# Performance work log

Hardware: AMD Instinct MI355X
Metric: run time of the kernel (lower is better)

The kernel has to match this reference:

```python
import jax, jax.numpy as jnp
import numpy as np

B, IN_F, N_HID = 2048, 512, 2048
HEAD = N_HID + IN_F  # 2560


def setup_inputs() -> dict:
    key = jax.random.key(0)
    ks = jax.random.split(key, 14)
    scale = 1.0 / np.sqrt(HEAD)
    # sparsity mask: original [IN_F, N_HID] in {-1,0,1}; _prep_mask pads with
    # ones [N_HID, N_HID], transposes, abs -> [N_HID, HEAD] of {0,1}
    raw = jax.random.randint(ks[0], (IN_F, N_HID), -1, 2).astype(jnp.float32)
    mask = jnp.abs(jnp.concatenate([raw, jnp.ones((N_HID, N_HID), jnp.float32)], axis=0).T)
    def w(k):
        return jax.random.normal(k, (N_HID, HEAD), jnp.float32) * scale
    def b(k):
        return jax.random.normal(k, (N_HID,), jnp.float32) * scale
    return {
        "x": jax.random.normal(ks[1], (B, IN_F), jnp.float32),
        "hidden": jax.random.normal(ks[2], (B, N_HID), jnp.float32),
        "mask": mask,
        "Wg": w(ks[3]), "bg": b(ks[4]),
        "Wh": w(ks[5]), "bh": b(ks[6]),
        "Wfg": w(ks[7]), "bfg": b(ks[8]),
        "Wfh": w(ks[9]), "bfh": b(ks[10]),
        "Wp": w(ks[11]), "bp": b(ks[12]),
    }


def reference(x, hidden, mask, Wg, bg, Wh, bh, Wfg, bfg, Wfh, bfh, Wp, bp):
    # concatenated input shared by all 5 masked linears: [B, HEAD]
    xc = jnp.concatenate([x, hidden], axis=1)
    # fuse the 5 masked GEMMs into one: [5, N_HID, HEAD] stacked weights
    W_all = jnp.stack([Wg, Wh, Wfg, Wfh, Wp]) * mask[None]
    b_all = jnp.stack([bg, bh, bfg, bfh, bp])
    outs = jnp.einsum('bh,koh->kbo', xc, W_all) + b_all[:, None, :]  # [5, B, N_HID]
    g_out, h_out, fg_out, fh_out, p_out = outs
    g = jnp.tanh(g_out)
    h = jnp.tanh(h_out)
    gate = jax.nn.sigmoid(fg_out + fh_out)
    new_hidden = g * (1.0 - gate) + gate * h
    y_pred = p_out + new_hidden
    return (y_pred, new_hidden)
```

## Files before the change

### kernel.cpp

```cpp
#include <hip/hip_runtime.h>

#define MDIM 2048
#define KD   2560
#define NHID 2048
#define INF  512
#define NS   40

typedef __attribute__((ext_vector_type(16))) float f32x16;
typedef __attribute__((ext_vector_type(8))) short short8;
typedef __attribute__((ext_vector_type(8))) unsigned short ushort8v;
typedef __attribute__((ext_vector_type(4))) unsigned short ushort4v;

#define AS1 __attribute__((address_space(1)))
#define AS3 __attribute__((address_space(3)))

__device__ __forceinline__ unsigned short f2bf(float f) {
    unsigned u = __float_as_uint(f);
    u += 0x7fffu + ((u >> 16) & 1u);
    return (unsigned short)(u >> 16);
}

#define XCB 2560
__global__ void prep_all(const float* __restrict__ x, const float* __restrict__ h,
                         unsigned short* __restrict__ xc,
                         const float* __restrict__ Wg, const float* __restrict__ Wh,
                         const float* __restrict__ Wfg, const float* __restrict__ Wfh,
                         const float* __restrict__ Wp, const float* __restrict__ mask,
                         unsigned short* __restrict__ Wm) {
    if (blockIdx.x < XCB) {
        int idx = blockIdx.x * 256 + threadIdx.x;
        int e = idx * 8;
        int b = e / KD;
        int c = e - b * KD;
        const float* src = (c < INF) ? (x + (size_t)b * INF + c)
                                     : (h + (size_t)b * NHID + (c - INF));
        float4 v0 = *(const float4*)src;
        float4 v1 = *(const float4*)(src + 4);
        ushort8v o;
        o[0] = f2bf(v0.x); o[1] = f2bf(v0.y); o[2] = f2bf(v0.z); o[3] = f2bf(v0.w);
        o[4] = f2bf(v1.x); o[5] = f2bf(v1.y); o[6] = f2bf(v1.z); o[7] = f2bf(v1.w);
        *(ushort8v*)(xc + e) = o;
    } else {
        int idx = (blockIdx.x - XCB) * 256 + threadIdx.x;
        size_t e = (size_t)idx * 4;
        const size_t PL = (size_t)NHID * KD;
        int col = (int)(e % KD);
        float4 m;
        if (col < INF) m = *(const float4*)(mask + e);
        else           m = make_float4(1.f, 1.f, 1.f, 1.f);
        const float* Ws[5] = {Wg, Wh, Wfg, Wfh, Wp};
        #pragma unroll
        for (int k = 0; k < 5; ++k) {
            float4 w = *(const float4*)(Ws[k] + e);
            ushort4v o;
            o[0] = f2bf(w.x * m.x); o[1] = f2bf(w.y * m.y);
            o[2] = f2bf(w.z * m.z); o[3] = f2bf(w.w * m.w);
            *(ushort4v*)(Wm + k * PL + e) = o;
        }
    }
}

#define MFMA32(d, va, vb) d = __builtin_amdgcn_mfma_f32_32x32x16_bf16(va, vb, d, 0, 0, 0)

__global__ __launch_bounds__(512, 2) void gemm_fused(
    const unsigned short* __restrict__ A,
    const unsigned short* __restrict__ Bm,
    const float* __restrict__ bg, const float* __restrict__ bh,
    const float* __restrict__ bfg, const float* __restrict__ bfh,
    const float* __restrict__ bp,
    float* __restrict__ out) {
    __shared__ unsigned short lsA[2][256 * 64];
    __shared__ unsigned short lsB[2][320 * 64];

    const int tid  = threadIdx.x;
    const int lane = tid & 63;
    const int w    = tid >> 6;
    const int wm   = w >> 1;
    const int wn   = w & 1;
    const int l31  = lane & 31;
    const int hi   = lane >> 5;
    const int l7   = lane & 7;
    const int u    = l31 >> 3;
    const int sc   = lane & 7;
    const int su   = lane >> 3;
    const int m0   = blockIdx.y * 256;
    const int n0c  = blockIdx.x * 64;

    const int ar0 = (w >> 2) * 128 + (w & 3) * 8;
    const int br0 = (w >> 1) * 80 + (w & 1) * 8;

    unsigned aOff[4], bOff[5];
    #pragma unroll
    for (int j = 0; j < 4; ++j) {
        const int r0 = ar0 + 32 * j;
        const int colv = ((sc ^ su ^ ((r0 >> 3) & 7)) << 3);
        aOff[j] = (unsigned)(((r0 + su) * KD + colv) * 2);
    }
    #pragma unroll
    for (int j = 0; j < 5; ++j) {
        const int r0 = br0 + 16 * j;
        const int grow = (r0 >> 6) * NHID + n0c + (r0 & 63);
        const int colv = ((sc ^ su ^ ((r0 >> 3) & 7)) << 3);
        bOff[j] = (unsigned)(((grow + su) * KD + colv) * 2);
    }
    const char* aBase = (const char*)A + (size_t)m0 * KD * 2;
    const char* bBase = (const char*)Bm;

#define STG(buf) do { \
        _Pragma("unroll") \
        for (int j = 0; j < 4; ++j) \
            __builtin_amdgcn_global_load_lds( \
                (const AS1 unsigned int*)(aBase + aOff[j]), \
                (AS3 unsigned int*)(&lsA[buf][(ar0 + 32 * j) * 64]), 16, 0, 0); \
        _Pragma("unroll") \
        for (int j = 0; j < 5; ++j) \
            __builtin_amdgcn_global_load_lds( \
                (const AS1 unsigned int*)(bBase + bOff[j]), \
                (AS3 unsigned int*)(&lsB[buf][(br0 + 16 * j) * 64]), 16, 0, 0); \
        aBase += 128; bBase += 128; \
    } while (0)

    const int arow = wm * 64 + l31;
    const int brow = wn * 32 + l31;
    const int keyB = (4 * wn + u) & 7;
    unsigned aRd[2][4], bRd[4];
    #pragma unroll
    for (int s = 0; s < 4; ++s) {
        #pragma unroll
        for (int m = 0; m < 2; ++m)
            aRd[m][s] = (unsigned)(((arow + 32 * m) * 64
                       + (((2 * s + hi) ^ l7 ^ ((4 * m + u) & 7)) << 3)) * 2);
        bRd[s] = (unsigned)((brow * 64 + (((2 * s + hi) ^ l7 ^ keyB) << 3)) * 2);
    }

    f32x16 acc[2][5] = {};

#define COMPUTE(bcl) do { \
        const char* baseA_ = (const char*)&lsA[bcl][0]; \
        const char* baseB_ = (const char*)&lsB[bcl][0]; \
        _Pragma("unroll") \
        for (int s = 0; s < 4; ++s) { \
            short8 av[2], bv[5]; \
            _Pragma("unroll") \
            for (int m = 0; m < 2; ++m) \
                av[m] = *(const short8*)(baseA_ + aRd[m][s]); \
            _Pragma("unroll") \
            for (int p = 0; p < 5; ++p) \
                bv[p] = *(const short8*)(baseB_ + bRd[s] + p * 8192); \
            __builtin_amdgcn_s_setprio(1); \
            _Pragma("unroll") \
            for (int m = 0; m < 2; ++m) \
                _Pragma("unroll") \
                for (int p = 0; p < 5; ++p) \
                    MFMA32(acc[m][p], av[m], bv[p]); \
            __builtin_amdgcn_s_setprio(0); \
        } \
    } while (0)

#define ENDBAR() do { \
        asm volatile("s_waitcnt vmcnt(0)" ::: "memory"); \
        __builtin_amdgcn_s_barrier(); \
    } while (0)

    STG(0);
    ENDBAR();

    for (int kt = 0; kt < NS; kt += 2) {
        STG(1);
        COMPUTE(0);
        ENDBAR();
        if (kt + 2 < NS) STG(0);
        COMPUTE(1);
        ENDBAR();
    }

    const int col = n0c + wn * 32 + l31;
    const float bgv = bg[col];
    const float bhv = bh[col];
    const float bfv = bfg[col] + bfh[col];
    const float bpv = bp[col];
    const size_t PL = (size_t)MDIM * NHID;
    #pragma unroll
    for (int m = 0; m < 2; ++m) {
        #pragma unroll
        for (int q = 0; q < 4; ++q) {
            #pragma unroll
            for (int t = 0; t < 4; ++t) {
                const int e = q * 4 + t;
                const int row = m0 + wm * 64 + m * 32 + q * 8 + 4 * hi + t;
                float gx = acc[m][0][e] + bgv;
                float hx = acc[m][1][e] + bhv;
                float sx = acc[m][2][e] + acc[m][3][e] + bfv;
                float tg = __expf(-2.0f * fabsf(gx));
                float g  = __builtin_copysignf((1.0f - tg) / (1.0f + tg), gx);
                float th = __expf(-2.0f * fabsf(hx));
                float hh = __builtin_copysignf((1.0f - th) / (1.0f + th), hx);
                float gate = 1.0f / (1.0f + __expf(-sx));
                float nh = g * (1.0f - gate) + gate * hh;
                float y  = acc[m][4][e] + bpv + nh;
                out[(size_t)row * NHID + col]      = y;
                out[PL + (size_t)row * NHID + col] = nh;
            }
        }
    }
#undef STG
#undef COMPUTE
#undef ENDBAR
}

extern "C" void kernel_launch(void* const* d_in, const int* in_sizes, int n_in,
                              void* d_out, int out_size, void* d_ws, size_t ws_size,
                              hipStream_t stream) {
    const float* x      = (const float*)d_in[0];
    const float* hidden = (const float*)d_in[1];
    const float* mask   = (const float*)d_in[2];
    const float* Wg     = (const float*)d_in[3];
    const float* bg     = (const float*)d_in[4];
    const float* Wh     = (const float*)d_in[5];
    const float* bh     = (const float*)d_in[6];
    const float* Wfg    = (const float*)d_in[7];
    const float* bfg    = (const float*)d_in[8];
    const float* Wfh    = (const float*)d_in[9];
    const float* bfh    = (const float*)d_in[10];
    const float* Wp     = (const float*)d_in[11];
    const float* bp     = (const float*)d_in[12];
    float* out = (float*)d_out;

    const size_t need = (size_t)MDIM * KD * 2 + (size_t)5 * NHID * KD * 2;
    if (ws_size < need) return;

    unsigned short* xc = (unsigned short*)d_ws;
    unsigned short* Wm = xc + (size_t)MDIM * KD;

    prep_all<<<XCB + NHID * KD / 4 / 256, 256, 0, stream>>>(
        x, hidden, xc, Wg, Wh, Wfg, Wfh, Wp, mask, Wm);
    dim3 grid(NHID / 64, MDIM / 256);
    gemm_fused<<<grid, 512, 0, stream>>>(xc, Wm, bg, bh, bfg, bfh, bp, out);
}
```

Baseline: 133.9 us.

## Software-pipeline LDS fragment reads with inline asm and lgkmcnt waits

Replaces the compiler-scheduled per-k-step LDS loads with hand-issued ds_read_b128 instructions into two register sets. The next k-step's fragments are loaded while MFMAs run on the current set, gated by partial lgkmcnt waits and sched barriers. Swizzled addresses are updated with XOR deltas instead of precomputed offset tables. The B buffers are split into two separate arrays so immediate offsets can be used. This aims to hide LDS latency behind MFMA issue, but it relies on the XOR address updates being correct and it raises register pressure.

```diff
diff --git a/kernel.cpp b/kernel.cpp
--- a/kernel.cpp
+++ b/kernel.cpp
@@ -8,6 +8,7 @@
 
 typedef __attribute__((ext_vector_type(16))) float f32x16;
 typedef __attribute__((ext_vector_type(8))) short short8;
+typedef __attribute__((ext_vector_type(4))) unsigned int u32x4;
 typedef __attribute__((ext_vector_type(8))) unsigned short ushort8v;
 typedef __attribute__((ext_vector_type(4))) unsigned short ushort4v;
 
@@ -62,6 +63,13 @@
 
 #define MFMA32(d, va, vb) d = __builtin_amdgcn_mfma_f32_32x32x16_bf16(va, vb, d, 0, 0, 0)
 
+#define DSR(dst, addr, OFS) \
+    asm volatile("ds_read_b128 %0, %1 offset:" OFS : "=v"(dst) : "v"(addr) : "memory")
+#define LGKM7 do { asm volatile("s_waitcnt lgkmcnt(7)" ::: "memory"); \
+                   __builtin_amdgcn_sched_barrier(0); } while (0)
+#define LGKM0 do { asm volatile("s_waitcnt lgkmcnt(0)" ::: "memory"); \
+                   __builtin_amdgcn_sched_barrier(0); } while (0)
+
 __global__ __launch_bounds__(512, 2) void gemm_fused(
     const unsigned short* __restrict__ A,
     const unsigned short* __restrict__ Bm,
@@ -70,7 +78,8 @@
     const float* __restrict__ bp,
     float* __restrict__ out) {
     __shared__ unsigned short lsA[2][256 * 64];
-    __shared__ unsigned short lsB[2][320 * 64];
+    __shared__ unsigned short lsB0[320 * 64];
+    __shared__ unsigned short lsB1[320 * 64];
 
     const int tid  = threadIdx.x;
     const int lane = tid & 63;
@@ -116,45 +125,45 @@
         for (int j = 0; j < 5; ++j) \
             __builtin_amdgcn_global_load_lds( \
                 (const AS1 unsigned int*)(bBase + bOff[j]), \
-                (AS3 unsigned int*)(&lsB[buf][(br0 + 16 * j) * 64]), 16, 0, 0); \
+                (AS3 unsigned int*)((buf) ? &lsB1[(br0 + 16 * j) * 64] \
+                                          : &lsB0[(br0 + 16 * j) * 64]), 16, 0, 0); \
         aBase += 128; bBase += 128; \
     } while (0)
 
     const int arow = wm * 64 + l31;
     const int brow = wn * 32 + l31;
     const int keyB = (4 * wn + u) & 7;
-    unsigned aRd[2][4], bRd[4];
-    #pragma unroll
-    for (int s = 0; s < 4; ++s) {
-        #pragma unroll
-        for (int m = 0; m < 2; ++m)
-            aRd[m][s] = (unsigned)(((arow + 32 * m) * 64
-                       + (((2 * s + hi) ^ l7 ^ ((4 * m + u) & 7)) << 3)) * 2);
-        bRd[s] = (unsigned)((brow * 64 + (((2 * s + hi) ^ l7 ^ keyB) << 3)) * 2);
-    }
+    unsigned aA0 = (unsigned)(size_t)(AS3 const unsigned short*)
+        &lsA[0][arow * 64 + ((hi ^ l7 ^ (u & 7)) << 3)];
+    unsigned aA1 = (unsigned)(size_t)(AS3 const unsigned short*)
+        &lsA[0][(arow + 32) * 64 + ((hi ^ l7 ^ ((4 + u) & 7)) << 3)];
+    unsigned bB0a = (unsigned)(size_t)(AS3 const unsigned short*)
+        &lsB0[brow * 64 + ((hi ^ l7 ^ keyB) << 3)];
+    unsigned bB1a = (unsigned)(size_t)(AS3 const unsigned short*)
+        &lsB1[brow * 64 + ((hi ^ l7 ^ keyB) << 3)];
+
+#define XUP(D) do { aA0 ^= (D); aA1 ^= (D); bB0a ^= (D); bB1a ^= (D); } while (0)
+
+#define ISSUE(SET, AOFS, BADDR) do { \
+        DSR(SET[0], aA0, AOFS); DSR(SET[1], aA1, AOFS); \
+        DSR(SET[2], BADDR, "0");     DSR(SET[3], BADDR, "8192"); \
+        DSR(SET[4], BADDR, "16384"); DSR(SET[5], BADDR, "24576"); \
+        DSR(SET[6], BADDR, "32768"); \
+    } while (0)
 
     f32x16 acc[2][5] = {};
 
-#define COMPUTE(bcl) do { \
-        const char* baseA_ = (const char*)&lsA[bcl][0]; \
-        const char* baseB_ = (const char*)&lsB[bcl][0]; \
+#define MM(SET) do { \
+        short8 a0_ = __builtin_bit_cast(short8, SET[0]); \
+        short8 a1_ = __builtin_bit_cast(short8, SET[1]); \
+        __builtin_amdgcn_s_setprio(1); \
         _Pragma("unroll") \
-        for (int s = 0; s < 4; ++s) { \
-            short8 av[2], bv[5]; \
-            _Pragma("unroll") \
-            for (int m = 0; m < 2; ++m) \
-                av[m] = *(const short8*)(baseA_ + aRd[m][s]); \
-            _Pragma("unroll") \
-            for (int p = 0; p < 5; ++p) \
-                bv[p] = *(const short8*)(baseB_ + bRd[s] + p * 8192); \
-            __builtin_amdgcn_s_setprio(1); \
-            _Pragma("unroll") \
-            for (int m = 0; m < 2; ++m) \
-                _Pragma("unroll") \
-                for (int p = 0; p < 5; ++p) \
-                    MFMA32(acc[m][p], av[m], bv[p]); \
-            __builtin_amdgcn_s_setprio(0); \
+        for (int p = 0; p < 5; ++p) { \
+            short8 bp_ = __builtin_bit_cast(short8, SET[2 + p]); \
+            MFMA32(acc[0][p], a0_, bp_); \
+            MFMA32(acc[1][p], a1_, bp_); \
         } \
+        __builtin_amdgcn_s_setprio(0); \
     } while (0)
 
 #define ENDBAR() do { \
@@ -162,16 +171,27 @@
         __builtin_amdgcn_s_barrier(); \
     } while (0)
 
+#define TILE(AOFS, BADDR, DO_STG, STGBUF) do { \
+        u32x4 fX[7], fY[7]; \
+        ISSUE(fX, AOFS, BADDR); \
+        if (DO_STG) STG(STGBUF); \
+        XUP(32); ISSUE(fY, AOFS, BADDR); \
+        LGKM7; MM(fX); \
+        XUP(96); ISSUE(fX, AOFS, BADDR); \
+        LGKM7; MM(fY); \
+        XUP(32); ISSUE(fY, AOFS, BADDR); \
+        LGKM7; MM(fX); \
+        XUP(96); \
+        LGKM0; MM(fY); \
+        ENDBAR(); \
+    } while (0)
+
     STG(0);
     ENDBAR();
 
     for (int kt = 0; kt < NS; kt += 2) {
-        STG(1);
-        COMPUTE(0);
-        ENDBAR();
-        if (kt + 2 < NS) STG(0);
-        COMPUTE(1);
-        ENDBAR();
+        TILE("0", bB0a, true, 1);
+        TILE("32768", bB1a, (kt + 2 < NS), 0);
     }
 
     const int col = n0c + wn * 32 + l31;
@@ -204,8 +224,11 @@
         }
     }
 #undef STG
-#undef COMPUTE
+#undef XUP
+#undef ISSUE
+#undef MM
 #undef ENDBAR
+#undef TILE
 }
 
 extern "C" void kernel_launch(void* const* d_in, const int* in_sizes, int n_in,
```

Result: slower. 170.2 us (+27.1%).

## Shrink GEMM block tile to 128 rows with 32-wide K slices

Applied to the files above, without the earlier changes.

Halves the block's M tile from 256 to 128 rows and the K slice from 64 to 32, with 256 threads per block instead of 512. The grid doubles, and the LDS swizzle plus the load and read offsets are redone for the 64-byte rows. The smaller LDS footprint should let more blocks sit on a CU and spread work across more blocks, which may hide latency better. The trade-offs are more barrier and K-loop iterations and twice as many global reads of the shared weight tile, since each B tile now serves only 128 rows.

```diff
diff --git a/kernel.cpp b/kernel.cpp
--- a/kernel.cpp
+++ b/kernel.cpp
@@ -4,7 +4,8 @@
 #define KD   2560
 #define NHID 2048
 #define INF  512
-#define NS   40
+#define BK   32
+#define NT   80
 
 typedef __attribute__((ext_vector_type(16))) float f32x16;
 typedef __attribute__((ext_vector_type(8))) short short8;
@@ -62,15 +63,15 @@
 
 #define MFMA32(d, va, vb) d = __builtin_amdgcn_mfma_f32_32x32x16_bf16(va, vb, d, 0, 0, 0)
 
-__global__ __launch_bounds__(512, 2) void gemm_fused(
+__global__ __launch_bounds__(256, 2) void gemm_fused(
     const unsigned short* __restrict__ A,
     const unsigned short* __restrict__ Bm,
     const float* __restrict__ bg, const float* __restrict__ bh,
     const float* __restrict__ bfg, const float* __restrict__ bfh,
     const float* __restrict__ bp,
     float* __restrict__ out) {
-    __shared__ unsigned short lsA[2][256 * 64];
-    __shared__ unsigned short lsB[2][320 * 64];
+    __shared__ unsigned short lsA[2][128 * BK];
+    __shared__ unsigned short lsB[2][320 * BK];
 
     const int tid  = threadIdx.x;
     const int lane = tid & 63;
@@ -79,58 +80,52 @@
     const int wn   = w & 1;
     const int l31  = lane & 31;
     const int hi   = lane >> 5;
-    const int l7   = lane & 7;
-    const int u    = l31 >> 3;
-    const int sc   = lane & 7;
-    const int su   = lane >> 3;
-    const int m0   = blockIdx.y * 256;
+    const int su   = lane >> 2;
+    const int sc   = lane & 3;
+    const int m0   = blockIdx.y * 128;
     const int n0c  = blockIdx.x * 64;
 
-    const int ar0 = (w >> 2) * 128 + (w & 3) * 8;
-    const int br0 = (w >> 1) * 80 + (w & 1) * 8;
-
-    unsigned aOff[4], bOff[5];
-    #pragma unroll
-    for (int j = 0; j < 4; ++j) {
-        const int r0 = ar0 + 32 * j;
-        const int colv = ((sc ^ su ^ ((r0 >> 3) & 7)) << 3);
-        aOff[j] = (unsigned)(((r0 + su) * KD + colv) * 2);
-    }
+    const int skey = sc ^ ((su ^ (su >> 2)) & 3);
+    const int ar0 = w * 32;
+    const int br0 = w * 80;
+
+    unsigned aOff[2], bOff[5];
+    #pragma unroll
+    for (int j = 0; j < 2; ++j)
+        aOff[j] = (unsigned)((((ar0 + 16 * j) + su) * KD + skey * 8) * 2);
     #pragma unroll
     for (int j = 0; j < 5; ++j) {
         const int r0 = br0 + 16 * j;
         const int grow = (r0 >> 6) * NHID + n0c + (r0 & 63);
-        const int colv = ((sc ^ su ^ ((r0 >> 3) & 7)) << 3);
-        bOff[j] = (unsigned)(((grow + su) * KD + colv) * 2);
+        bOff[j] = (unsigned)(((grow + su) * KD + skey * 8) * 2);
     }
     const char* aBase = (const char*)A + (size_t)m0 * KD * 2;
     const char* bBase = (const char*)Bm;
 
 #define STG(buf) do { \
         _Pragma("unroll") \
-        for (int j = 0; j < 4; ++j) \
+        for (int j = 0; j < 2; ++j) \
             __builtin_amdgcn_global_load_lds( \
                 (const AS1 unsigned int*)(aBase + aOff[j]), \
-                (AS3 unsigned int*)(&lsA[buf][(ar0 + 32 * j) * 64]), 16, 0, 0); \
+                (AS3 unsigned int*)(&lsA[buf][(ar0 + 16 * j) * BK]), 16, 0, 0); \
         _Pragma("unroll") \
         for (int j = 0; j < 5; ++j) \
             __builtin_amdgcn_global_load_lds( \
                 (const AS1 unsigned int*)(bBase + bOff[j]), \
-                (AS3 unsigned int*)(&lsB[buf][(br0 + 16 * j) * 64]), 16, 0, 0); \
-        aBase += 128; bBase += 128; \
+                (AS3 unsigned int*)(&lsB[buf][(br0 + 16 * j) * BK]), 16, 0, 0); \
+        aBase += 64; bBase += 64; \
     } while (0)
 
     const int arow = wm * 64 + l31;
     const int brow = wn * 32 + l31;
-    const int keyB = (4 * wn + u) & 7;
-    unsigned aRd[2][4], bRd[4];
-    #pragma unroll
-    for (int s = 0; s < 4; ++s) {
+    const int kk = (l31 ^ (l31 >> 2)) & 3;
+    unsigned aRd[2][2], bRd[2];
+    #pragma unroll
+    for (int s = 0; s < 2; ++s) {
         #pragma unroll
         for (int m = 0; m < 2; ++m)
-            aRd[m][s] = (unsigned)(((arow + 32 * m) * 64
-                       + (((2 * s + hi) ^ l7 ^ ((4 * m + u) & 7)) << 3)) * 2);
-        bRd[s] = (unsigned)((brow * 64 + (((2 * s + hi) ^ l7 ^ keyB) << 3)) * 2);
+            aRd[m][s] = (unsigned)((arow + 32 * m) * 64 + (((2 * s + hi) ^ kk) << 4));
+        bRd[s] = (unsigned)(brow * 64 + (((2 * s + hi) ^ kk) << 4));
     }
 
     f32x16 acc[2][5] = {};
@@ -139,14 +134,14 @@
         const char* baseA_ = (const char*)&lsA[bcl][0]; \
         const char* baseB_ = (const char*)&lsB[bcl][0]; \
         _Pragma("unroll") \
-        for (int s = 0; s < 4; ++s) { \
+        for (int s = 0; s < 2; ++s) { \
             short8 av[2], bv[5]; \
             _Pragma("unroll") \
             for (int m = 0; m < 2; ++m) \
                 av[m] = *(const short8*)(baseA_ + aRd[m][s]); \
             _Pragma("unroll") \
             for (int p = 0; p < 5; ++p) \
-                bv[p] = *(const short8*)(baseB_ + bRd[s] + p * 8192); \
+                bv[p] = *(const short8*)(baseB_ + bRd[s] + p * 4096); \
             __builtin_amdgcn_s_setprio(1); \
             _Pragma("unroll") \
             for (int m = 0; m < 2; ++m) \
@@ -165,11 +160,11 @@
     STG(0);
     ENDBAR();
 
-    for (int kt = 0; kt < NS; kt += 2) {
+    for (int kt = 0; kt < NT; kt += 2) {
         STG(1);
         COMPUTE(0);
         ENDBAR();
-        if (kt + 2 < NS) STG(0);
+        if (kt + 2 < NT) STG(0);
         COMPUTE(1);
         ENDBAR();
     }
@@ -234,6 +229,6 @@
 
     prep_all<<<XCB + NHID * KD / 4 / 256, 256, 0, stream>>>(
         x, hidden, xc, Wg, Wh, Wfg, Wfh, Wp, mask, Wm);
-    dim3 grid(NHID / 64, MDIM / 256);
-    gemm_fused<<<grid, 512, 0, stream>>>(xc, Wm, bg, bh, bfg, bfh, bp, out);
-}
+    dim3 grid(NHID / 64, MDIM / 128);
+    gemm_fused<<<grid, 256, 0, stream>>>(xc, Wm, bg, bh, bfg, bfh, bp, out);
+}
```

Measured after the change: 151.6 us. 13.2% more time.
